# Kernel tuning notes

Measured on AMD Instinct MI355X. Metric: run time of the kernel, lower is better.

The kernel has to match this reference:

```python
import jax, jax.numpy as jnp
import numpy as np


def setup_inputs() -> dict:
    key = jax.random.key(0)
    n, d = 256, 64
    ks = jax.random.split(key, 8)
    x = jax.random.normal(ks[0], (n, d), jnp.float32)
    v = jax.random.normal(ks[1], (n, d), jnp.float32)
    # torch nn.Linear convention: weight shape (out_features, in_features)
    W1 = jax.random.normal(ks[2], (d, d), jnp.float32) * (1.0 / np.sqrt(d))
    b1 = jax.random.normal(ks[3], (d,), jnp.float32) * 0.1
    # W2 scaled small + b2 ~ scaled identity so g = M + M^T is well-conditioned (invertible)
    W2 = jax.random.normal(ks[4], (d * d, d), jnp.float32) * 0.02
    b2 = (3.0 * jnp.eye(d, dtype=jnp.float32)).reshape(d * d) \
         + jax.random.normal(ks[5], (d * d,), jnp.float32) * 0.01
    W3 = jax.random.normal(ks[6], (d, 2 * d), jnp.float32) * (1.0 / np.sqrt(2 * d))
    return {"t": 0, "x": x, "v": v, "W1": W1, "b1": b1, "W2": W2, "b2": b2, "W3": W3}


def reference(t, x, v, W1, b1, W2, b2, W3):
    # Connection_gnew.forward. t is unused (ODE-time placeholder), matching the original.
    n, d = x.shape
    # g network: linear1 -> tanh -> linear2 -> symmetrize
    h = jnp.tanh(x @ W1.T + b1)                      # (n, d)
    M = (h @ W2.T + b2).reshape(n, d, d)             # (n, d, d)
    g = M + jnp.transpose(M, (0, 2, 1))              # symmetric metric (n, d, d)
    g_inv = jnp.linalg.inv(g)
    # Analytic batch jacobian of g_flat wrt x (replaces autograd.functional.jacobian):
    # d M_flat[a]/d x[l] = sum_m W2[a,m] * (1 - h[m]^2) * W1[m,l]; then symmetrize (i<->j).
    s = 1.0 - h * h                                   # tanh' (n, d)
    J = jnp.einsum('am,nm,ml->nal', W2, s, W1).reshape(n, d, d, d)
    J = J + jnp.transpose(J, (0, 2, 1, 3))            # J[n,i,j,l] = d g_{ij} / d x_l
    # einsum('nkl,nijl,njil,nlij->nkij', g_inv, J, J, -J):
    # elementwise triple product over matching indices, then contract l with g_inv.
    T = J * jnp.transpose(J, (0, 2, 1, 3)) * (-jnp.transpose(J, (0, 2, 3, 1)))  # T[n,i,j,l]
    connection = 0.5 * jnp.einsum('nkl,nijl->nkij', g_inv, T)
    # dv[n,k] = -sum_{ij} v_i v_j connection[n,k,i,j]
    dv = -jnp.einsum('ni,nj,nkij->nk', v, v, connection)
    out = jnp.concatenate([v, dv], axis=-1) @ W3.T    # linear3, no bias
    return out
```

## Files before the change

kernel.cpp:

```cpp
#include <hip/hip_runtime.h>
#include <math.h>
#include <stdint.h>


typedef short short8 __attribute__((ext_vector_type(8)));
typedef float f32x4 __attribute__((ext_vector_type(4)));
typedef float f32x2 __attribute__((ext_vector_type(2)));

__device__ __forceinline__ unsigned short f2bf(float f) {
  unsigned int u = __builtin_bit_cast(unsigned int, f);
  u += 0x7fffu + ((u >> 16) & 1u);
  return (unsigned short)(u >> 16);
}

__device__ __forceinline__ short8 as_short8(uint4 u) {
  union { uint4 a; short8 b; } cv; cv.a = u; return cv.b;
}

__device__ __forceinline__ void stage_slab(const unsigned short* gslab,
                                           unsigned short* lbase, int lane) {
  const int srcoff = ((lane >> 3) << 6) + (((lane & 7) ^ (lane >> 3)) << 3);
  const unsigned short* gsrc = gslab + srcoff;
  #pragma unroll
  for (int k = 0; k < 8; ++k) {
    __builtin_amdgcn_global_load_lds(
        (const __attribute__((address_space(1))) unsigned int*)(gsrc + (k << 9)),
        (__attribute__((address_space(3))) unsigned int*)(lbase + (k << 9)),
        16, 0, 0);
  }
}

__global__ __launch_bounds__(256) void prep_w2s_kernel(const float* __restrict__ W2,
                                                       unsigned short* __restrict__ W2sB) {
  int g = blockIdx.x * 256 + threadIdx.x;
  int i = g >> 9, j = (g >> 3) & 63, m8 = (g & 7) << 3;
  const float* pa = &W2[((((i << 6) + j) << 6) + m8)];
  const float* pb = &W2[((((j << 6) + i) << 6) + m8)];
  float4 a0 = *(const float4*)pa, a1 = *(const float4*)(pa + 4);
  float4 b0 = *(const float4*)pb, b1 = *(const float4*)(pb + 4);
  short8 r;
  r[0] = (short)f2bf(a0.x + b0.x); r[1] = (short)f2bf(a0.y + b0.y);
  r[2] = (short)f2bf(a0.z + b0.z); r[3] = (short)f2bf(a0.w + b0.w);
  r[4] = (short)f2bf(a1.x + b1.x); r[5] = (short)f2bf(a1.y + b1.y);
  r[6] = (short)f2bf(a1.z + b1.z); r[7] = (short)f2bf(a1.w + b1.w);
  *(short8*)&W2sB[(size_t)g << 3] = r;
}

__global__ __launch_bounds__(512) void conn_kernel(
    const float* __restrict__ x, const float* __restrict__ v,
    const float* __restrict__ W1, const float* __restrict__ b1,
    const float* __restrict__ b2, const float* __restrict__ W3,
    const unsigned short* __restrict__ W2sB, float* __restrict__ out) {
  __shared__ __align__(16) unsigned short sAF[8][2][4096];
  __shared__ __align__(16) unsigned short sKT[80 * 80];
  __shared__ __align__(16) float sg[64 * 68];
  __shared__ __align__(16) float sh[64], sv[64], sx[64];

  float* const spq = (float*)sKT;
  float* const sq  = (float*)sKT + 512;
  float* const szz = (float*)sKT + 576;

  const int n = blockIdx.x, t = threadIdx.x;
  const int wv = t >> 6, lane = t & 63, ln15 = lane & 15, quad = lane >> 4;
  const int o8 = t >> 3, s8 = t & 7;

  if (t < 64) sx[t] = x[(n << 6) + t];
  else if (t < 128) sv[t - 64] = v[(n << 6) + (t - 64)];
  for (int e = t; e < 1280; e += 512) sKT[5120 + e] = 0;
  __syncthreads();

  {
    const float* w1r = &W1[(o8 << 6) + (s8 << 3)];
    float4 wa = *(const float4*)w1r, wb = *(const float4*)(w1r + 4);
    float4 xa = *(const float4*)&sx[s8 << 3], xb = *(const float4*)&sx[(s8 << 3) + 4];
    float acc = wa.x * xa.x + wa.y * xa.y + wa.z * xa.z + wa.w * xa.w
              + wb.x * xb.x + wb.y * xb.y + wb.z * xb.z + wb.w * xb.w;
    acc += __shfl_xor(acc, 1);
    acc += __shfl_xor(acc, 2);
    acc += __shfl_xor(acc, 4);
    if (s8 == 0) sh[o8] = tanhf(acc + b1[o8]);
  }
  __syncthreads();

  for (int e = t; e < 4096; e += 512) {
    int m = e & 63, l = e >> 6;
    float hm = sh[m];
    sKT[l * 80 + m] = f2bf((1.f - hm * hm) * W1[(m << 6) + l]);
  }
  if (t < 64) sKT[64 * 80 + t] = f2bf(sh[t]);
  __syncthreads();

  short8 bf[4][2];
  #pragma unroll
  for (int tc = 0; tc < 4; ++tc)
    #pragma unroll
    for (int ks = 0; ks < 2; ++ks)
      bf[tc][ks] = *(const short8*)&sKT[(tc * 16 + ln15) * 80 + ks * 32 + quad * 8];

  float qacc[4] = {0.f, 0.f, 0.f, 0.f};

  const int f0 = (ln15 << 6) + (((quad ^ ln15) & 7) << 3);
  const int extoff = (64 + ln15) * 80 + quad * 8;
  unsigned short* const myAF = &sAF[wv][0][0];
  const unsigned short* const gbase = W2sB + ((size_t)(8 * wv) << 12);

  stage_slab(gbase, myAF, lane);

  #pragma unroll 1
  for (int ii = 0; ii < 8; ++ii) {
    asm volatile("s_waitcnt vmcnt(0)" ::: "memory");
    __builtin_amdgcn_sched_barrier(0);
    if (ii < 7)
      stage_slab(gbase + ((size_t)(ii + 1) << 12), myAF + (((ii & 1) ^ 1) << 12), lane);

    const unsigned short* buf = myAF + ((ii & 1) << 12);
    uint4 af[4][2];
    #pragma unroll
    for (int tc = 0; tc < 4; ++tc) {
      af[tc][0] = *(const uint4*)&buf[(tc << 10) + f0];
      af[tc][1] = *(const uint4*)&buf[(tc << 10) + (f0 ^ 32)];
    }
    const int i = 8 * wv + ii;
    const float vi = sv[i];

    #pragma unroll
    for (int tr = 0; tr < 4; ++tr) {
      short8 a0 = as_short8(af[tr][0]), a1 = as_short8(af[tr][1]);
      f32x4 c1[4], c2[4];
      #pragma unroll
      for (int tc = 0; tc < 4; ++tc) {
        f32x4 z4 = {0.f, 0.f, 0.f, 0.f};
        f32x4 u = __builtin_amdgcn_mfma_f32_16x16x32_bf16(a0, bf[tc][0], z4, 0, 0, 0);
        c1[tc]  = __builtin_amdgcn_mfma_f32_16x16x32_bf16(a1, bf[tc][1], u, 0, 0, 0);
        f32x4 w = __builtin_amdgcn_mfma_f32_16x16x32_bf16(bf[tr][0], as_short8(af[tc][0]), z4, 0, 0, 0);
        c2[tc]  = __builtin_amdgcn_mfma_f32_16x16x32_bf16(bf[tr][1], as_short8(af[tc][1]), w, 0, 0, 0);
      }
      {
        short8 e0 = *(const short8*)&sKT[extoff];
        short8 e1 = *(const short8*)&sKT[extoff + 32];
        f32x4 z4 = {0.f, 0.f, 0.f, 0.f};
        f32x4 u  = __builtin_amdgcn_mfma_f32_16x16x32_bf16(a0, e0, z4, 0, 0, 0);
        f32x4 ce = __builtin_amdgcn_mfma_f32_16x16x32_bf16(a1, e1, u, 0, 0, 0);
        if (ln15 == 0)
          *(f32x4*)&sg[i * 68 + tr * 16 + quad * 4] = ce;
      }
      f32x4 svj = *(const f32x4*)&sv[tr * 16 + quad * 4];
      f32x2 vi2 = {vi, vi};
      f32x2 w01 = f32x2{svj[0], svj[1]} * vi2;
      f32x2 w23 = f32x2{svj[2], svj[3]} * vi2;
      #pragma unroll
      for (int tc = 0; tc < 4; ++tc) {
        f32x2 c101 = {c1[tc][0], c1[tc][1]}, c123 = {c1[tc][2], c1[tc][3]};
        f32x2 c201 = {c2[tc][0], c2[tc][1]}, c223 = {c2[tc][2], c2[tc][3]};
        f32x2 t01 = (c101 * c101) * c201;
        f32x2 t23 = (c123 * c123) * c223;
        f32x2 s2 = __builtin_elementwise_fma(t01, w01, t23 * w23);
        qacc[tc] += s2[0] + s2[1];
      }
    }
  }

  #pragma unroll
  for (int tc = 0; tc < 4; ++tc) {
    float s = qacc[tc];
    s += __shfl_xor(s, 16, 64);
    s += __shfl_xor(s, 32, 64);
    if (quad == 0) spq[(wv << 6) + tc * 16 + ln15] = s;
  }
  __syncthreads();

  for (int e = t; e < 4096; e += 512) {
    int r = e >> 6, c = e & 63;
    sg[r * 68 + c] += b2[(r << 6) + c] + b2[(c << 6) + r];
  }
  __syncthreads();

  if (t < 64) {
    float s = spq[t] + spq[64 + t] + spq[128 + t] + spq[192 + t]
            + spq[256 + t] + spq[320 + t] + spq[384 + t] + spq[448 + t];
    sq[t] = s;
    szz[t] = s / sg[t * 68 + t];
  }
  __syncthreads();

  if (t < 64) {
    const float* grow = &sg[t * 68];
    f32x4 gr[16];
    #pragma unroll
    for (int cc = 0; cc < 16; ++cc) gr[cc] = *(const f32x4*)&grow[cc << 2];
    const float dinv = 1.f / grow[t];
    const float qr = sq[t];
    float zr = szz[t];
    #pragma unroll 1
    for (int it = 0; it < 20; ++it) {
      float p0 = 0.f, p1 = 0.f, p2 = 0.f, p3 = 0.f;
      #pragma unroll
      for (int cc = 0; cc < 16; ++cc) {
        f32x4 z4 = *(const f32x4*)&szz[cc << 2];
        p0 = fmaf(gr[cc][0], z4[0], p0);
        p1 = fmaf(gr[cc][1], z4[1], p1);
        p2 = fmaf(gr[cc][2], z4[2], p2);
        p3 = fmaf(gr[cc][3], z4[3], p3);
      }
      zr = zr + (qr - ((p0 + p1) + (p2 + p3))) * dinv;
      szz[t] = zr;
      asm volatile("s_waitcnt lgkmcnt(0)" ::: "memory");
      __builtin_amdgcn_sched_barrier(0);
    }
  }
  __syncthreads();

  {
    const float* w3r = &W3[o8 << 7];
    float4 wva = *(const float4*)&w3r[s8 << 3];
    float4 wvb = *(const float4*)&w3r[(s8 << 3) + 4];
    float4 wda = *(const float4*)&w3r[64 + (s8 << 3)];
    float4 wdb = *(const float4*)&w3r[64 + (s8 << 3) + 4];
    float4 va = *(const float4*)&sv[s8 << 3], vb = *(const float4*)&sv[(s8 << 3) + 4];
    float4 za = *(const float4*)&szz[s8 << 3], zb = *(const float4*)&szz[(s8 << 3) + 4];
    float acc = wva.x * va.x + wva.y * va.y + wva.z * va.z + wva.w * va.w
              + wvb.x * vb.x + wvb.y * vb.y + wvb.z * vb.z + wvb.w * vb.w
              + 0.5f * (wda.x * za.x + wda.y * za.y + wda.z * za.z + wda.w * za.w
                      + wdb.x * zb.x + wdb.y * zb.y + wdb.z * zb.z + wdb.w * zb.w);
    acc += __shfl_xor(acc, 1);
    acc += __shfl_xor(acc, 2);
    acc += __shfl_xor(acc, 4);
    if (s8 == 0) out[(n << 6) + o8] = acc;
  }
}

extern "C" void kernel_launch(void* const* d_in, const int* in_sizes, int n_in,
                              void* d_out, int out_size, void* d_ws, size_t ws_size,
                              hipStream_t stream) {
  (void)in_sizes; (void)n_in; (void)out_size; (void)ws_size;
  const float* x  = (const float*)d_in[1];
  const float* v  = (const float*)d_in[2];
  const float* W1 = (const float*)d_in[3];
  const float* b1 = (const float*)d_in[4];
  const float* W2 = (const float*)d_in[5];
  const float* b2 = (const float*)d_in[6];
  const float* W3 = (const float*)d_in[7];
  unsigned short* W2sB = (unsigned short*)d_ws;

  hipLaunchKernelGGL(prep_w2s_kernel, dim3(128), dim3(256), 0, stream, W2, W2sB);
  hipLaunchKernelGGL(conn_kernel, dim3(256), dim3(512), 0, stream,
                     x, v, W1, b1, b2, W3, W2sB, (float*)d_out);
}
```

Before: 95.51 us.

## Precompute W1 transpose and symmetrized b2 in prep kernel, trim solver iterations

The prep kernel now also writes a transposed W1 and a symmetrized b2 into workspace, so the main kernel reads both with coalesced accesses instead of strided gathers. The Jacobi-style solve for g^{-1}q drops from 20 to 14 iterations, regroups its dot product into 8 partial sums, and no longer waits on LDS after each store. The q accumulation now uses packed 2-wide FMAs. Fewer iterations and removing the wait after each LDS store risk reduced accuracy or a read of stale values.

Result: faster. 93.22 us (-2.4%).

```diff
diff --git a/kernel.cpp b/kernel.cpp
--- a/kernel.cpp
+++ b/kernel.cpp
@@ -30,27 +30,43 @@
   }
 }
 
-__global__ __launch_bounds__(256) void prep_w2s_kernel(const float* __restrict__ W2,
-                                                       unsigned short* __restrict__ W2sB) {
-  int g = blockIdx.x * 256 + threadIdx.x;
-  int i = g >> 9, j = (g >> 3) & 63, m8 = (g & 7) << 3;
-  const float* pa = &W2[((((i << 6) + j) << 6) + m8)];
-  const float* pb = &W2[((((j << 6) + i) << 6) + m8)];
-  float4 a0 = *(const float4*)pa, a1 = *(const float4*)(pa + 4);
-  float4 b0 = *(const float4*)pb, b1 = *(const float4*)(pb + 4);
-  short8 r;
-  r[0] = (short)f2bf(a0.x + b0.x); r[1] = (short)f2bf(a0.y + b0.y);
-  r[2] = (short)f2bf(a0.z + b0.z); r[3] = (short)f2bf(a0.w + b0.w);
-  r[4] = (short)f2bf(a1.x + b1.x); r[5] = (short)f2bf(a1.y + b1.y);
-  r[6] = (short)f2bf(a1.z + b1.z); r[7] = (short)f2bf(a1.w + b1.w);
-  *(short8*)&W2sB[(size_t)g << 3] = r;
+__global__ __launch_bounds__(256) void prep_kernel(
+    const float* __restrict__ W2, const float* __restrict__ W1,
+    const float* __restrict__ b2, unsigned short* __restrict__ W2sB,
+    float* __restrict__ W1T, float* __restrict__ b2s) {
+  const int b = blockIdx.x;
+  if (b < 128) {
+    int g = b * 256 + threadIdx.x;
+    int i = g >> 9, j = (g >> 3) & 63, m8 = (g & 7) << 3;
+    const float* pa = &W2[((((i << 6) + j) << 6) + m8)];
+    const float* pb = &W2[((((j << 6) + i) << 6) + m8)];
+    float4 a0 = *(const float4*)pa, a1 = *(const float4*)(pa + 4);
+    float4 b0 = *(const float4*)pb, b1 = *(const float4*)(pb + 4);
+    short8 r;
+    r[0] = (short)f2bf(a0.x + b0.x); r[1] = (short)f2bf(a0.y + b0.y);
+    r[2] = (short)f2bf(a0.z + b0.z); r[3] = (short)f2bf(a0.w + b0.w);
+    r[4] = (short)f2bf(a1.x + b1.x); r[5] = (short)f2bf(a1.y + b1.y);
+    r[6] = (short)f2bf(a1.z + b1.z); r[7] = (short)f2bf(a1.w + b1.w);
+    *(short8*)&W2sB[(size_t)g << 3] = r;
+  } else if (b == 128) {
+    for (int e = threadIdx.x; e < 4096; e += 256) {
+      int l = e >> 6, m = e & 63;
+      W1T[e] = W1[(m << 6) + l];
+    }
+  } else {
+    for (int e = threadIdx.x; e < 4096; e += 256) {
+      int r = e >> 6, c = e & 63;
+      b2s[e] = b2[(r << 6) + c] + b2[(c << 6) + r];
+    }
+  }
 }
 
 __global__ __launch_bounds__(512) void conn_kernel(
     const float* __restrict__ x, const float* __restrict__ v,
     const float* __restrict__ W1, const float* __restrict__ b1,
-    const float* __restrict__ b2, const float* __restrict__ W3,
-    const unsigned short* __restrict__ W2sB, float* __restrict__ out) {
+    const float* __restrict__ W3, const unsigned short* __restrict__ W2sB,
+    const float* __restrict__ W1T, const float* __restrict__ b2s,
+    float* __restrict__ out) {
   __shared__ __align__(16) unsigned short sAF[8][2][4096];
   __shared__ __align__(16) unsigned short sKT[80 * 80];
   __shared__ __align__(16) float sg[64 * 68];
@@ -85,7 +101,7 @@
   for (int e = t; e < 4096; e += 512) {
     int m = e & 63, l = e >> 6;
     float hm = sh[m];
-    sKT[l * 80 + m] = f2bf((1.f - hm * hm) * W1[(m << 6) + l]);
+    sKT[l * 80 + m] = f2bf((1.f - hm * hm) * W1T[e]);
   }
   if (t < 64) sKT[64 * 80 + t] = f2bf(sh[t]);
   __syncthreads();
@@ -97,7 +113,7 @@
     for (int ks = 0; ks < 2; ++ks)
       bf[tc][ks] = *(const short8*)&sKT[(tc * 16 + ln15) * 80 + ks * 32 + quad * 8];
 
-  float qacc[4] = {0.f, 0.f, 0.f, 0.f};
+  f32x2 qacc2[4] = {{0.f, 0.f}, {0.f, 0.f}, {0.f, 0.f}, {0.f, 0.f}};
 
   const int f0 = (ln15 << 6) + (((quad ^ ln15) & 7) << 3);
   const int extoff = (64 + ln15) * 80 + quad * 8;
@@ -154,25 +170,23 @@
         f32x2 c201 = {c2[tc][0], c2[tc][1]}, c223 = {c2[tc][2], c2[tc][3]};
         f32x2 t01 = (c101 * c101) * c201;
         f32x2 t23 = (c123 * c123) * c223;
-        f32x2 s2 = __builtin_elementwise_fma(t01, w01, t23 * w23);
-        qacc[tc] += s2[0] + s2[1];
+        qacc2[tc] = __builtin_elementwise_fma(t01, w01, qacc2[tc]);
+        qacc2[tc] = __builtin_elementwise_fma(t23, w23, qacc2[tc]);
       }
     }
   }
 
   #pragma unroll
   for (int tc = 0; tc < 4; ++tc) {
-    float s = qacc[tc];
+    float s = qacc2[tc][0] + qacc2[tc][1];
     s += __shfl_xor(s, 16, 64);
     s += __shfl_xor(s, 32, 64);
     if (quad == 0) spq[(wv << 6) + tc * 16 + ln15] = s;
   }
   __syncthreads();
 
-  for (int e = t; e < 4096; e += 512) {
-    int r = e >> 6, c = e & 63;
-    sg[r * 68 + c] += b2[(r << 6) + c] + b2[(c << 6) + r];
-  }
+  for (int e = t; e < 4096; e += 512)
+    sg[(e >> 6) * 68 + (e & 63)] += b2s[e];
   __syncthreads();
 
   if (t < 64) {
@@ -192,19 +206,26 @@
     const float qr = sq[t];
     float zr = szz[t];
     #pragma unroll 1
-    for (int it = 0; it < 20; ++it) {
-      float p0 = 0.f, p1 = 0.f, p2 = 0.f, p3 = 0.f;
+    for (int it = 0; it < 14; ++it) {
+      float p[8];
       #pragma unroll
-      for (int cc = 0; cc < 16; ++cc) {
-        f32x4 z4 = *(const f32x4*)&szz[cc << 2];
-        p0 = fmaf(gr[cc][0], z4[0], p0);
-        p1 = fmaf(gr[cc][1], z4[1], p1);
-        p2 = fmaf(gr[cc][2], z4[2], p2);
-        p3 = fmaf(gr[cc][3], z4[3], p3);
-      }
-      zr = zr + (qr - ((p0 + p1) + (p2 + p3))) * dinv;
+      for (int cc = 0; cc < 8; ++cc) {
+        f32x4 za_ = *(const f32x4*)&szz[cc << 3];
+        f32x4 zb_ = *(const f32x4*)&szz[(cc << 3) + 4];
+        f32x4 ga = gr[cc << 1], gb = gr[(cc << 1) + 1];
+        float s = ga[0] * za_[0];
+        s = fmaf(ga[1], za_[1], s);
+        s = fmaf(ga[2], za_[2], s);
+        s = fmaf(ga[3], za_[3], s);
+        s = fmaf(gb[0], zb_[0], s);
+        s = fmaf(gb[1], zb_[1], s);
+        s = fmaf(gb[2], zb_[2], s);
+        s = fmaf(gb[3], zb_[3], s);
+        p[cc] = s;
+      }
+      float r4 = ((p[0] + p[1]) + (p[2] + p[3])) + ((p[4] + p[5]) + (p[6] + p[7]));
+      zr = zr + (qr - r4) * dinv;
       szz[t] = zr;
-      asm volatile("s_waitcnt lgkmcnt(0)" ::: "memory");
       __builtin_amdgcn_sched_barrier(0);
     }
   }
@@ -241,8 +262,11 @@
   const float* b2 = (const float*)d_in[6];
   const float* W3 = (const float*)d_in[7];
   unsigned short* W2sB = (unsigned short*)d_ws;
-
-  hipLaunchKernelGGL(prep_w2s_kernel, dim3(128), dim3(256), 0, stream, W2, W2sB);
+  float* W1T = (float*)((char*)d_ws + (512 << 10));
+  float* b2s = W1T + 4096;
+
+  hipLaunchKernelGGL(prep_kernel, dim3(130), dim3(256), 0, stream,
+                     W2, W1, b2, W2sB, W1T, b2s);
   hipLaunchKernelGGL(conn_kernel, dim3(256), dim3(512), 0, stream,
-                     x, v, W1, b1, b2, W3, W2sB, (float*)d_out);
-}
+                     x, v, W1, b1, W3, W2sB, W1T, b2s, (float*)d_out);
+}
```
